# Optimization experiments

Measured on AMD Instinct MI355X. Metric: run time of the kernel, lower is better.

The kernel has to match this reference:

```python
import jax, jax.numpy as jnp
import numpy as np

NB = 31      # num_bands
PD = 64      # processing_dim


def _conv(x, w, b, groups, pad):
    # x: NCHW, w: OIHW (I = in_channels/groups)
    y = jax.lax.conv_general_dilated(
        x, w, window_strides=(1, 1), padding=pad,
        feature_group_count=groups,
        dimension_numbers=('NCHW', 'OIHW', 'NCHW'))
    return y + b[None, :, None, None]


def _gelu(z):
    # torch.nn.GELU() default is exact (erf-based)
    return jax.nn.gelu(z, approximate=False)


def setup_inputs() -> dict:
    key = jax.random.key(0)
    ks = jax.random.split(key, 11)
    s = 0.05
    inp = {
        'x':   jax.random.normal(ks[0], (2, NB, 192, 192), dtype=jnp.float32),
        # 31 independent band processors, stacked as grouped-conv weights (groups=31)
        'W1':  jax.random.normal(ks[1], (NB * PD, 1, 3, 3), dtype=jnp.float32) * s,
        'b1':  jax.random.normal(ks[2], (NB * PD,), dtype=jnp.float32) * s,
        'W2':  jax.random.normal(ks[3], (NB * PD, PD, 3, 3), dtype=jnp.float32) * s,
        'b2':  jax.random.normal(ks[4], (NB * PD,), dtype=jnp.float32) * s,
        'W3':  jax.random.normal(ks[5], (NB, PD, 1, 1), dtype=jnp.float32) * s,
        'b3':  jax.random.normal(ks[6], (NB,), dtype=jnp.float32) * s,
        # cross-band fusion 1x1 convs
        'Wf1': jax.random.normal(ks[7], (NB * 2, NB, 1, 1), dtype=jnp.float32) * s,
        'bf1': jax.random.normal(ks[8], (NB * 2,), dtype=jnp.float32) * s,
        'Wf2': jax.random.normal(ks[9], (NB, NB * 2, 1, 1), dtype=jnp.float32) * s,
        'bf2': jax.random.normal(ks[10], (NB,), dtype=jnp.float32) * s,
    }
    return inp


def reference(x, W1, b1, W2, b2, W3, b3, Wf1, bf1, Wf2, bf2):
    P3 = [(1, 1), (1, 1)]
    P1 = [(0, 0), (0, 0)]
    # per-band 3-layer stacks expressed as grouped convs (groups = num_bands)
    h = _gelu(_conv(x, W1, b1, NB, P3))           # [B, 31*64, H, W]
    h = _gelu(_conv(h, W2, b2, NB, P3))           # [B, 31*64, H, W]
    processed = _conv(h, W3, b3, NB, P1)          # [B, 31, H, W]
    # cross-band fusion
    f = _gelu(_conv(processed, Wf1, bf1, 1, P1))  # [B, 62, H, W]
    fused = _conv(f, Wf2, bf2, 1, P1)             # [B, 31, H, W]
    return x + fused
```

## Files before the change

### kernel.cpp

```cpp
#include <hip/hip_runtime.h>
#include <hip/hip_bf16.h>

#define NB 31
#define PD 64

typedef __attribute__((ext_vector_type(8))) short short8;
typedef __attribute__((ext_vector_type(16))) float f32x16;
typedef __attribute__((ext_vector_type(8))) int int8v;

__device__ __forceinline__ float gelu_f(float x) {
    float y = x * x;
    float p = __builtin_fmaf(y, __builtin_fmaf(y, 0.0042294f, -0.056913f), 0.395442f);
    float phi;
    asm("v_fma_f32 %0, %1, %2, 0.5 clamp" : "=v"(phi) : "v"(x), "v"(p));
    return x * phi;
}

__device__ __forceinline__ unsigned int cvt_pk_bf16(float lo, float hi) {
    unsigned int r;
    asm("v_cvt_pk_bf16_f32 %0, %1, %2" : "=v"(r) : "v"(lo), "v"(hi));
    return r;
}

__device__ __forceinline__ unsigned int pk_fp8(float a, float b) {
    return (unsigned int)__builtin_amdgcn_cvt_pk_fp8_f32(a, b, 0, false);
}

__device__ __forceinline__ int8v mk8(uint4 a, uint4 b) {
    int8v r;
    r[0] = a.x; r[1] = a.y; r[2] = a.z; r[3] = a.w;
    r[4] = b.x; r[5] = b.y; r[6] = b.z; r[7] = b.w;
    return r;
}

__global__ void prep_w2(const float* __restrict__ W2, unsigned char* __restrict__ W2s) {
    int e = blockIdx.x * 256 + threadIdx.x;
    const int TOT = NB * 2 * 9 * 64;
    if (e >= TOT) return;
    int lane = e & 63;
    int tap  = (e >> 6) % 9;
    int gh   = e / (9 * 64);
    int g = gh >> 1, oh = gh & 1;
    int col = lane & 31, hi = lane >> 5;
    const float* wp = W2 + ((size_t)(g * 64 + oh * 32 + col) * 64 + hi * 32) * 9 + tap;
    unsigned int d[8];
#pragma unroll
    for (int i = 0; i < 8; ++i) {
        float f0 = wp[(4 * i + 0) * 9];
        float f1 = wp[(4 * i + 1) * 9];
        float f2 = wp[(4 * i + 2) * 9];
        float f3 = wp[(4 * i + 3) * 9];
        d[i] = pk_fp8(f0, f1) | (pk_fp8(f2, f3) << 16);
    }
    uint4 q0, q1;
    q0.x = d[0]; q0.y = d[2]; q0.z = d[4]; q0.w = d[6];
    q1.x = d[1]; q1.y = d[3]; q1.z = d[5]; q1.w = d[7];
    uint4* op = (uint4*)W2s + (size_t)e * 2;
    op[0] = q0; op[1] = q1;
}

__global__ __launch_bounds__(512, 4) void band_kernel(
    const float* __restrict__ x, const float* __restrict__ W1, const float* __restrict__ b1,
    const float* __restrict__ b2, const float* __restrict__ W3, const float* __restrict__ b3,
    const unsigned char* __restrict__ W2s, float* __restrict__ out)
{
    __shared__ float xs[20 * 36];
    __shared__ uint4 h1s[704 * 5];
    __shared__ float outs[2 * 256];

    const int tid = threadIdx.x;
    const int txp = blockIdx.x % 6, ty = blockIdx.x / 6;
    const int g = blockIdx.y, n = blockIdx.z;
    const int x0c = txp * 32, y0 = ty * 16;

    const int lane = tid & 63;
    const int wid  = tid >> 6;
    const int w4   = wid & 3;
    const int oh   = wid >> 2;
    const int hi   = lane >> 5;
    const int col  = lane & 31;

    const float* xg = x + (size_t)(n * NB + g) * 192 * 192;
    for (int i = tid; i < 720; i += 512) {
        int r = i / 36, c = i - r * 36;
        int gy = y0 + r - 2, gx = x0c + c - 2;
        float v = 0.f;
        if (gy >= 0 && gy < 192 && gx >= 0 && gx < 192) v = xg[gy * 192 + gx];
        xs[i] = v;
    }

    short8 a1;
    {
        const float* wp = W1 + (size_t)(g * 64 + oh * 32 + col) * 9;
        uint4 bw = {0u, 0u, 0u, 0u};
        if (hi == 0) {
            bw.x = cvt_pk_bf16(wp[0], wp[1]);
            bw.y = cvt_pk_bf16(wp[2], wp[3]);
            bw.z = cvt_pk_bf16(wp[4], wp[5]);
            bw.w = cvt_pk_bf16(wp[6], wp[7]);
        } else {
            bw.x = cvt_pk_bf16(wp[8], b1[g * 64 + oh * 32 + col]);
        }
        a1 = __builtin_bit_cast(short8, bw);
    }
    __syncthreads();

    char* h1c = (char*)h1s;
    const int lhalf = (lane >> 4) & 1;
    const int pxl   = lane & 15;
    const int base0 = (4 * w4 + lhalf) * 18 + pxl;
    const int gh = g * 2 + oh;
    const uint4* ap = (const uint4*)W2s + (size_t)gh * 9 * 128 + lane * 2;

    auto conv1_iter = [&](int T, int it) {
        const int t = w4 + 4 * it;
        if (t < 11) {
            const int posr = t * 32 + col;
            const int pos  = posr < 324 ? posr : 323;
            int py = pos / 18, px = pos - py * 18;
            int gy = y0 + py - 1, gx = x0c + T * 16 + px - 1;
            unsigned int msk = (gy >= 0 && gy < 192 && gx >= 0 && gx < 192) ? 0xFFFFFFFFu : 0u;

            uint4 bw = {0u, 0u, 0u, 0u};
            if (hi == 0) {
                float xv[8];
#pragma unroll
                for (int j2 = 0; j2 < 8; ++j2)
                    xv[j2] = xs[(py + j2 / 3) * 36 + T * 16 + px + (j2 % 3)];
                bw.x = cvt_pk_bf16(xv[0], xv[1]);
                bw.y = cvt_pk_bf16(xv[2], xv[3]);
                bw.z = cvt_pk_bf16(xv[4], xv[5]);
                bw.w = cvt_pk_bf16(xv[6], xv[7]);
            } else {
                bw.x = cvt_pk_bf16(xs[(py + 2) * 36 + T * 16 + px + 2], 1.0f);
            }
            short8 bfrag = __builtin_bit_cast(short8, bw);

            f32x16 z = {};
            f32x16 c0 = __builtin_amdgcn_mfma_f32_32x32x16_bf16(a1, bfrag, z, 0, 0, 0);

            uint4 st;
            {
                float u0 = gelu_f(c0[0]),  u1 = gelu_f(c0[1]);
                float u2 = gelu_f(c0[2]),  u3 = gelu_f(c0[3]);
                st.x = (pk_fp8(u0, u1) | (pk_fp8(u2, u3) << 16)) & msk;
            }
            {
                float u0 = gelu_f(c0[4]),  u1 = gelu_f(c0[5]);
                float u2 = gelu_f(c0[6]),  u3 = gelu_f(c0[7]);
                st.y = (pk_fp8(u0, u1) | (pk_fp8(u2, u3) << 16)) & msk;
            }
            {
                float u0 = gelu_f(c0[8]),  u1 = gelu_f(c0[9]);
                float u2 = gelu_f(c0[10]), u3 = gelu_f(c0[11]);
                st.z = (pk_fp8(u0, u1) | (pk_fp8(u2, u3) << 16)) & msk;
            }
            {
                float u0 = gelu_f(c0[12]), u1 = gelu_f(c0[13]);
                float u2 = gelu_f(c0[14]), u3 = gelu_f(c0[15]);
                st.w = (pk_fp8(u0, u1) | (pk_fp8(u2, u3) << 16)) & msk;
            }
            *(uint4*)(h1c + T * 28160 + posr * 80 + (oh << 5) + (hi << 4)) = st;
        }
    };

    auto acc_init = [&](f32x16& A0v, f32x16& A1v) {
        const float* bp = b2 + g * 64 + oh * 32 + 4 * hi;
#pragma unroll
        for (int s = 0; s < 4; ++s) {
            float4 q = *(const float4*)(bp + 8 * s);
            A0v[4 * s + 0] = q.x; A0v[4 * s + 1] = q.y;
            A0v[4 * s + 2] = q.z; A0v[4 * s + 3] = q.w;
            A1v[4 * s + 0] = q.x; A1v[4 * s + 1] = q.y;
            A1v[4 * s + 2] = q.z; A1v[4 * s + 3] = q.w;
        }
    };

    auto conv2_taps = [&](int T, int tap0, f32x16& A0v, f32x16& A1v) {
#pragma unroll
        for (int tt = 0; tt < 3; ++tt) {
            const int tap = tap0 + tt;
            const int D = (tap / 3) * 18 + (tap % 3);
            const int p0 = base0 + D;
            const int p1 = p0 + 36;
            const char* r0 = h1c + T * 28160 + p0 * 80 + (hi << 5);
            const char* r1 = h1c + T * 28160 + p1 * 80 + (hi << 5);
            uint4 b0a = *(const uint4*)(r0);
            uint4 b0b = *(const uint4*)(r0 + 16);
            uint4 b1a = *(const uint4*)(r1);
            uint4 b1b = *(const uint4*)(r1 + 16);
            uint4 al = ap[tap * 128], ah = ap[tap * 128 + 1];
            int8v A = mk8(al, ah);
            A0v = __builtin_amdgcn_mfma_scale_f32_32x32x64_f8f6f4(
                      A, mk8(b0a, b0b), A0v, 0, 0, 0, 0x7F7F7F7F, 0, 0x7F7F7F7F);
            A1v = __builtin_amdgcn_mfma_scale_f32_32x32x64_f8f6f4(
                      A, mk8(b1a, b1b), A1v, 0, 0, 0, 0x7F7F7F7F, 0, 0x7F7F7F7F);
        }
    };

    auto epilogue = [&](f32x16& A0v, f32x16& A1v) {
        float pa = 0.f, pb = 0.f;
        const float* wp3 = W3 + g * 64 + oh * 32 + 4 * hi;
#pragma unroll
        for (int s = 0; s < 4; ++s) {
            float4 qa = *(const float4*)(wp3 + 8 * s);
            pa = __builtin_fmaf(qa.x, gelu_f(A0v[4 * s + 0]), pa);
            pa = __builtin_fmaf(qa.y, gelu_f(A0v[4 * s + 1]), pa);
            pa = __builtin_fmaf(qa.z, gelu_f(A0v[4 * s + 2]), pa);
            pa = __builtin_fmaf(qa.w, gelu_f(A0v[4 * s + 3]), pa);
            pb = __builtin_fmaf(qa.x, gelu_f(A1v[4 * s + 0]), pb);
            pb = __builtin_fmaf(qa.y, gelu_f(A1v[4 * s + 1]), pb);
            pb = __builtin_fmaf(qa.z, gelu_f(A1v[4 * s + 2]), pb);
            pb = __builtin_fmaf(qa.w, gelu_f(A1v[4 * s + 3]), pb);
        }
        pa += __shfl_xor(pa, 32);
        pb += __shfl_xor(pb, 32);
        if (lane < 32) {
            outs[oh * 256 + w4 * 64 + lane]      = pa;
            outs[oh * 256 + w4 * 64 + 32 + lane] = pb;
        }
    };

    auto outwrite = [&](int T) {
        if (tid < 256) {
            float v = outs[tid] + outs[256 + tid] + b3[g];
            int py_ = 4 * (tid >> 6) + 2 * ((tid >> 5) & 1) + ((tid >> 4) & 1);
            int px_ = tid & 15;
            out[((size_t)(n * NB + g) * 192 + y0 + py_) * 192 + x0c + T * 16 + px_] = v;
        }
    };

    conv1_iter(0, 0); conv1_iter(0, 1); conv1_iter(0, 2);
    __syncthreads();

    f32x16 acc0, acc1;
    acc_init(acc0, acc1);
    conv1_iter(1, 0); conv2_taps(0, 0, acc0, acc1);
    conv1_iter(1, 1); conv2_taps(0, 3, acc0, acc1);
    conv1_iter(1, 2); conv2_taps(0, 6, acc0, acc1);
    epilogue(acc0, acc1);
    __syncthreads();
    outwrite(0);
    __syncthreads();

    acc_init(acc0, acc1);
    conv2_taps(1, 0, acc0, acc1);
    conv2_taps(1, 3, acc0, acc1);
    conv2_taps(1, 6, acc0, acc1);
    epilogue(acc0, acc1);
    __syncthreads();
    outwrite(1);
}

__global__ __launch_bounds__(512) void fuse_kernel(
    const float* __restrict__ x,
    const float* __restrict__ Wf1, const float* __restrict__ bf1,
    const float* __restrict__ Wf2, const float* __restrict__ bf2,
    float* __restrict__ out)
{
    __shared__ float part[256 * 33];
    const int tid  = threadIdx.x;
    const int half = __builtin_amdgcn_readfirstlane(tid >> 8);
    const int pixl = tid & 255;
    int p = blockIdx.x * 256 + pixl;
    int nn = p / 36864, pix = p - nn * 36864;
    float* basep = out + (size_t)nn * NB * 36864 + pix;
    const float* xb = x + (size_t)nn * NB * 36864 + pix;

    float v[31];
#pragma unroll
    for (int c = 0; c < 31; ++c) v[c] = basep[(size_t)c * 36864];

    float fused[31];
#pragma unroll
    for (int c = 0; c < 31; ++c) fused[c] = 0.f;

    for (int jj = 0; jj < 31; ++jj) {
        int j = half * 31 + jj;
        float a = bf1[j];
#pragma unroll
        for (int c = 0; c < 31; ++c) a = __builtin_fmaf(Wf1[j * 31 + c], v[c], a);
        float fj = gelu_f(a);
#pragma unroll
        for (int c = 0; c < 31; ++c) fused[c] = __builtin_fmaf(Wf2[c * 62 + j], fj, fused[c]);
    }

    if (half == 1) {
#pragma unroll
        for (int c = 0; c < 31; ++c) part[pixl * 33 + c] = fused[c];
    }
    __syncthreads();
    if (half == 0) {
#pragma unroll
        for (int c = 0; c < 31; ++c)
            basep[(size_t)c * 36864] =
                xb[(size_t)c * 36864] + fused[c] + part[pixl * 33 + c] + bf2[c];
    }
}

extern "C" void kernel_launch(void* const* d_in, const int* in_sizes, int n_in,
                              void* d_out, int out_size, void* d_ws, size_t ws_size,
                              hipStream_t stream) {
    const float* x   = (const float*)d_in[0];
    const float* W1  = (const float*)d_in[1];
    const float* b1  = (const float*)d_in[2];
    const float* W2  = (const float*)d_in[3];
    const float* b2  = (const float*)d_in[4];
    const float* W3  = (const float*)d_in[5];
    const float* b3  = (const float*)d_in[6];
    const float* Wf1 = (const float*)d_in[7];
    const float* bf1 = (const float*)d_in[8];
    const float* Wf2 = (const float*)d_in[9];
    const float* bf2 = (const float*)d_in[10];
    float* out = (float*)d_out;
    unsigned char* W2s = (unsigned char*)d_ws;

    const int TOT = NB * 2 * 9 * 64;
    hipLaunchKernelGGL(prep_w2, dim3((TOT + 255) / 256), dim3(256), 0, stream, W2, W2s);
    hipLaunchKernelGGL(band_kernel, dim3(72, NB, 2), dim3(512), 0, stream,
                       x, W1, b1, b2, W3, b3, W2s, out);
    hipLaunchKernelGGL(fuse_kernel, dim3(288), dim3(512), 0, stream,
                       x, Wf1, bf1, Wf2, bf2, out);
}
```

Before: 157.8 us.

## Widen band tile to 64 columns with double-buffered conv1 staging

Each band_kernel block now covers 64 output columns (four 16-wide strips) instead of 32, which halves the grid. The layer-1 activations are staged in a two-slot ring buffer in shared memory. The layer-1 conv for the next strip overlaps the layer-2 MFMA work on the current strip across all four strips. A double-buffered output staging area removes one barrier per strip. This amortises the halo load of x and the per-block W1/bias setup over more work and keeps the pipeline full for longer, but fewer blocks means less parallelism to hide tail effects.

```diff
diff --git a/kernel.cpp b/kernel.cpp
--- a/kernel.cpp
+++ b/kernel.cpp
@@ -64,14 +64,14 @@
     const float* __restrict__ b2, const float* __restrict__ W3, const float* __restrict__ b3,
     const unsigned char* __restrict__ W2s, float* __restrict__ out)
 {
-    __shared__ float xs[20 * 36];
-    __shared__ uint4 h1s[704 * 5];
-    __shared__ float outs[2 * 256];
+    __shared__ float xs[20 * 68];
+    __shared__ uint4 h1s[2][324 * 5];
+    __shared__ float outs[2][512];
 
     const int tid = threadIdx.x;
-    const int txp = blockIdx.x % 6, ty = blockIdx.x / 6;
+    const int txp = blockIdx.x % 3, ty = blockIdx.x / 3;
     const int g = blockIdx.y, n = blockIdx.z;
-    const int x0c = txp * 32, y0 = ty * 16;
+    const int x0c = txp * 64, y0 = ty * 16;
 
     const int lane = tid & 63;
     const int wid  = tid >> 6;
@@ -81,8 +81,8 @@
     const int col  = lane & 31;
 
     const float* xg = x + (size_t)(n * NB + g) * 192 * 192;
-    for (int i = tid; i < 720; i += 512) {
-        int r = i / 36, c = i - r * 36;
+    for (int i = tid; i < 1360; i += 512) {
+        int r = i / 68, c = i - r * 68;
         int gy = y0 + r - 2, gx = x0c + c - 2;
         float v = 0.f;
         if (gy >= 0 && gy < 192 && gx >= 0 && gx < 192) v = xg[gy * 192 + gx];
@@ -105,7 +105,6 @@
     }
     __syncthreads();
 
-    char* h1c = (char*)h1s;
     const int lhalf = (lane >> 4) & 1;
     const int pxl   = lane & 15;
     const int base0 = (4 * w4 + lhalf) * 18 + pxl;
@@ -126,13 +125,13 @@
                 float xv[8];
 #pragma unroll
                 for (int j2 = 0; j2 < 8; ++j2)
-                    xv[j2] = xs[(py + j2 / 3) * 36 + T * 16 + px + (j2 % 3)];
+                    xv[j2] = xs[(py + j2 / 3) * 68 + T * 16 + px + (j2 % 3)];
                 bw.x = cvt_pk_bf16(xv[0], xv[1]);
                 bw.y = cvt_pk_bf16(xv[2], xv[3]);
                 bw.z = cvt_pk_bf16(xv[4], xv[5]);
                 bw.w = cvt_pk_bf16(xv[6], xv[7]);
             } else {
-                bw.x = cvt_pk_bf16(xs[(py + 2) * 36 + T * 16 + px + 2], 1.0f);
+                bw.x = cvt_pk_bf16(xs[(py + 2) * 68 + T * 16 + px + 2], 1.0f);
             }
             short8 bfrag = __builtin_bit_cast(short8, bw);
 
@@ -160,7 +159,8 @@
                 float u2 = gelu_f(c0[14]), u3 = gelu_f(c0[15]);
                 st.w = (pk_fp8(u0, u1) | (pk_fp8(u2, u3) << 16)) & msk;
             }
-            *(uint4*)(h1c + T * 28160 + posr * 80 + (oh << 5) + (hi << 4)) = st;
+            if (posr < 324)
+                *(uint4*)((char*)h1s[T & 1] + posr * 80 + (oh << 5) + (hi << 4)) = st;
         }
     };
 
@@ -177,14 +177,15 @@
     };
 
     auto conv2_taps = [&](int T, int tap0, f32x16& A0v, f32x16& A1v) {
+        const char* hb = (const char*)h1s[T & 1];
 #pragma unroll
         for (int tt = 0; tt < 3; ++tt) {
             const int tap = tap0 + tt;
             const int D = (tap / 3) * 18 + (tap % 3);
             const int p0 = base0 + D;
             const int p1 = p0 + 36;
-            const char* r0 = h1c + T * 28160 + p0 * 80 + (hi << 5);
-            const char* r1 = h1c + T * 28160 + p1 * 80 + (hi << 5);
+            const char* r0 = hb + p0 * 80 + (hi << 5);
+            const char* r1 = hb + p1 * 80 + (hi << 5);
             uint4 b0a = *(const uint4*)(r0);
             uint4 b0b = *(const uint4*)(r0 + 16);
             uint4 b1a = *(const uint4*)(r1);
@@ -198,7 +199,7 @@
         }
     };
 
-    auto epilogue = [&](f32x16& A0v, f32x16& A1v) {
+    auto epilogue = [&](int b, f32x16& A0v, f32x16& A1v) {
         float pa = 0.f, pb = 0.f;
         const float* wp3 = W3 + g * 64 + oh * 32 + 4 * hi;
 #pragma unroll
@@ -216,14 +217,14 @@
         pa += __shfl_xor(pa, 32);
         pb += __shfl_xor(pb, 32);
         if (lane < 32) {
-            outs[oh * 256 + w4 * 64 + lane]      = pa;
-            outs[oh * 256 + w4 * 64 + 32 + lane] = pb;
-        }
-    };
-
-    auto outwrite = [&](int T) {
+            outs[b][oh * 256 + w4 * 64 + lane]      = pa;
+            outs[b][oh * 256 + w4 * 64 + 32 + lane] = pb;
+        }
+    };
+
+    auto outwrite = [&](int T, int b) {
         if (tid < 256) {
-            float v = outs[tid] + outs[256 + tid] + b3[g];
+            float v = outs[b][tid] + outs[b][256 + tid] + b3[g];
             int py_ = 4 * (tid >> 6) + 2 * ((tid >> 5) & 1) + ((tid >> 4) & 1);
             int px_ = tid & 15;
             out[((size_t)(n * NB + g) * 192 + y0 + py_) * 192 + x0c + T * 16 + px_] = v;
@@ -234,22 +235,38 @@
     __syncthreads();
 
     f32x16 acc0, acc1;
+
     acc_init(acc0, acc1);
     conv1_iter(1, 0); conv2_taps(0, 0, acc0, acc1);
     conv1_iter(1, 1); conv2_taps(0, 3, acc0, acc1);
     conv1_iter(1, 2); conv2_taps(0, 6, acc0, acc1);
-    epilogue(acc0, acc1);
-    __syncthreads();
-    outwrite(0);
-    __syncthreads();
+    epilogue(0, acc0, acc1);
+    __syncthreads();
+    outwrite(0, 0);
 
     acc_init(acc0, acc1);
-    conv2_taps(1, 0, acc0, acc1);
-    conv2_taps(1, 3, acc0, acc1);
-    conv2_taps(1, 6, acc0, acc1);
-    epilogue(acc0, acc1);
-    __syncthreads();
-    outwrite(1);
+    conv1_iter(2, 0); conv2_taps(1, 0, acc0, acc1);
+    conv1_iter(2, 1); conv2_taps(1, 3, acc0, acc1);
+    conv1_iter(2, 2); conv2_taps(1, 6, acc0, acc1);
+    epilogue(1, acc0, acc1);
+    __syncthreads();
+    outwrite(1, 1);
+
+    acc_init(acc0, acc1);
+    conv1_iter(3, 0); conv2_taps(2, 0, acc0, acc1);
+    conv1_iter(3, 1); conv2_taps(2, 3, acc0, acc1);
+    conv1_iter(3, 2); conv2_taps(2, 6, acc0, acc1);
+    epilogue(0, acc0, acc1);
+    __syncthreads();
+    outwrite(2, 0);
+
+    acc_init(acc0, acc1);
+    conv2_taps(3, 0, acc0, acc1);
+    conv2_taps(3, 3, acc0, acc1);
+    conv2_taps(3, 6, acc0, acc1);
+    epilogue(1, acc0, acc1);
+    __syncthreads();
+    outwrite(3, 1);
 }
 
 __global__ __launch_bounds__(512) void fuse_kernel(
@@ -317,7 +334,7 @@
 
     const int TOT = NB * 2 * 9 * 64;
     hipLaunchKernelGGL(prep_w2, dim3((TOT + 255) / 256), dim3(256), 0, stream, W2, W2s);
-    hipLaunchKernelGGL(band_kernel, dim3(72, NB, 2), dim3(512), 0, stream,
+    hipLaunchKernelGGL(band_kernel, dim3(36, NB, 2), dim3(512), 0, stream,
                        x, W1, b1, b2, W3, b3, W2s, out);
     hipLaunchKernelGGL(fuse_kernel, dim3(288), dim3(512), 0, stream,
                        x, Wf1, bf1, Wf2, bf2, out);
```

Measured after the change: 161.5 us. +2.3%, slower.
